# Optimization experiments

Measured on AMD Instinct MI355X. Metric: run time of the kernel, lower is better.

Reference implementation:

```python
import jax, jax.numpy as jnp
import numpy as np
import math

B, S, DM, H = 2, 2048, 1024, 16
DH = DM // H  # 64


def setup_inputs() -> dict:
    key = jax.random.key(0)
    ks = jax.random.split(key, 12)
    s = 1.0 / math.sqrt(DM)
    inp = {
        "key": jax.random.normal(ks[0], (B, S, DM), jnp.float32),
        "value": jax.random.normal(ks[1], (B, S, DM), jnp.float32),
        "query": jax.random.normal(ks[2], (B, S, DM), jnp.float32),
        # causal mask: True = masked out (matches masked_fill semantics)
        "mask": jnp.broadcast_to(~jnp.tril(jnp.ones((S, S), bool)), (B, S, S)),
        "Wk": jax.random.normal(ks[3], (DM, DM), jnp.float32) * s,
        "bk": jnp.zeros((DM,), jnp.float32),
        "Wv": jax.random.normal(ks[4], (DM, DM), jnp.float32) * s,
        "bv": jnp.zeros((DM,), jnp.float32),
        "Wq": jax.random.normal(ks[5], (DM, DM), jnp.float32) * s,
        "bq": jnp.zeros((DM,), jnp.float32),
        "Wo": jax.random.normal(ks[6], (DM, DM), jnp.float32) * s,
        "bo": jnp.zeros((DM,), jnp.float32),
    }
    return inp


def _split_heads(x):
    # [B, S, H*DH] -> [B, H, S, DH]
    b, s, _ = x.shape
    return x.reshape(b, s, H, DH).transpose(0, 2, 1, 3)


def reference(key, value, query, mask, Wk, bk, Wv, bv, Wq, bq, Wo, bo):
    key_up = _split_heads(key @ Wk.T + bk)      # [B,H,S,DH]
    value_up = _split_heads(value @ Wv.T + bv)  # [B,H,S,DH]
    query_up = _split_heads(query @ Wq.T + bq) / math.sqrt(DH)
    scores = jnp.einsum("bhqd,bhkd->bhqk", query_up, key_up)  # [B,H,S,S]
    scores = jnp.where(mask[:, None, :, :], jnp.float32(-1e18), scores)
    attn = jax.nn.softmax(scores, axis=-1)
    # dropout is identity in eval mode
    context = jnp.einsum("bhqk,bhkd->bhqd", attn, value_up)
    context = context.transpose(0, 2, 1, 3).reshape(key.shape[0], -1, H * DH)
    output = context @ Wo.T + bo                # [B,S,DM]
    top_attn = attn[:, 0, :, :]                 # [B,S,S]
    return output, top_attn
```

## Files before the change

### kernel.cpp

```cpp
#include <hip/hip_runtime.h>
#include <hip/hip_bf16.h>
#include <math.h>

#define B_ 2
#define S_ 2048
#define DM_ 1024
#define H_ 16
#define DH_ 64

using short8 = __attribute__((ext_vector_type(8))) short;
using f32x4  = __attribute__((ext_vector_type(4))) float;

typedef const __attribute__((address_space(1))) void* gas_cvp;
typedef __attribute__((address_space(3))) void* las_vp;

struct CvtJobs {
    const float* in[7];
    ushort* out[7];
    int n[7];
};

__device__ __forceinline__ ushort f2bu(float x) {
    __hip_bfloat16 h = __float2bfloat16(x);
    return *(ushort*)&h;
}

__global__ __launch_bounds__(256) void cvt_bf16(CvtJobs jobs) {
    const int j = blockIdx.y;
    const int n = jobs.n[j];
    const int idx = (blockIdx.x * 256 + threadIdx.x) * 8;
    if (idx >= n) return;
    const float* in = jobs.in[j];
    float4 a = *(const float4*)&in[idx];
    float4 b = *(const float4*)&in[idx + 4];
    ushort u[8];
    u[0] = f2bu(a.x); u[1] = f2bu(a.y); u[2] = f2bu(a.z); u[3] = f2bu(a.w);
    u[4] = f2bu(b.x); u[5] = f2bu(b.y); u[6] = f2bu(b.z); u[7] = f2bu(b.w);
    *(int4*)&jobs.out[j][idx] = *(int4*)u;
}

#define GEMM_STAGE(buf, k0v)                                                   \
    {                                                                          \
        _Pragma("unroll")                                                      \
        for (int i = 0; i < 2; i++) {                                          \
            const int s   = i * 256 + tid;                                     \
            const int c   = s >> 7;                                            \
            const int row = s & 127;                                           \
            __builtin_amdgcn_global_load_lds(                                  \
                (gas_cvp)(Ag + (size_t)(i0 + row) * 1024 + (k0v) + c * 8),     \
                (las_vp)&AsB[buf][0][(i * 256 + w * 64) * 8], 16, 0, 0);       \
            __builtin_amdgcn_global_load_lds(                                  \
                (gas_cvp)(Wg + (size_t)(j0 + row) * 1024 + (k0v) + c * 8),     \
                (las_vp)&AsB[buf][1][(i * 256 + w * 64) * 8], 16, 0, 0);       \
        }                                                                      \
    }

#define GEMM_KLOOP()                                                           \
    {                                                                          \
        int bufc = 0;                                                          \
        GEMM_STAGE(0, 0);                                                      \
        GEMM_STAGE(1, 32);                                                     \
        for (int k0 = 0; k0 < 1024; k0 += 32) {                                \
            if (k0 + 32 < 1024)                                                \
                asm volatile("s_waitcnt vmcnt(4)" ::: "memory");               \
            else                                                               \
                asm volatile("s_waitcnt vmcnt(0)" ::: "memory");               \
            __builtin_amdgcn_s_barrier();                                      \
            if (k0 + 64 < 1024) {                                              \
                const int nb = (bufc + 2 >= 3) ? bufc - 1 : bufc + 2;          \
                GEMM_STAGE(nb, k0 + 64);                                       \
            }                                                                  \
            short8 af[4], bf[4];                                               \
            _Pragma("unroll")                                                  \
            for (int m = 0; m < 4; m++)                                        \
                af[m] = *(const short8*)&AsB[bufc][0][((g << 7) + wm * 64 + m * 16 + lr) * 8]; \
            _Pragma("unroll")                                                  \
            for (int n = 0; n < 4; n++)                                        \
                bf[n] = *(const short8*)&AsB[bufc][1][((g << 7) + wn * 64 + n * 16 + lr) * 8]; \
            _Pragma("unroll")                                                  \
            for (int m = 0; m < 4; m++)                                        \
                _Pragma("unroll")                                              \
                for (int n = 0; n < 4; n++)                                    \
                    acc[m][n] = __builtin_amdgcn_mfma_f32_16x16x32_bf16(       \
                        af[m], bf[n], acc[m][n], 0, 0, 0);                     \
            bufc = (bufc + 1 == 3) ? 0 : bufc + 1;                             \
        }                                                                      \
    }

struct ProjJobs {
    const ushort* A[3];
    const ushort* W[3];
    const float* bias[3];
    ushort* C[3];
    float scale[3];
};

__global__ __launch_bounds__(256) void gemm_proj3(ProjJobs jobs)
{
    __shared__ ushort AsB[3][2][4096];

    const int o   = blockIdx.x;
    const int swz = (o & 7) * 96 + (o >> 3);
    const int z   = swz >> 8;
    const int rem = swz & 255;
    const int by  = rem >> 3;
    const int bx  = rem & 7;

    const ushort* Ag = jobs.A[z];
    const ushort* Wg = jobs.W[z];
    const float* bias = jobs.bias[z];
    ushort* C = jobs.C[z];
    const float scale = jobs.scale[z];

    const int tid  = threadIdx.x;
    const int w    = tid >> 6;
    const int lane = tid & 63;
    const int g    = lane >> 4;
    const int lr   = lane & 15;
    const int wm   = w >> 1;
    const int wn   = w & 1;
    const int i0   = by * 128;
    const int j0   = bx * 128;

    f32x4 acc[4][4];
    #pragma unroll
    for (int m = 0; m < 4; m++)
        #pragma unroll
        for (int n = 0; n < 4; n++)
            #pragma unroll
            for (int jj = 0; jj < 4; jj++) acc[m][n][jj] = 0.f;

    GEMM_KLOOP();

    const int colbase = j0 + wn * 64;
    const int rowbase = i0 + wm * 64;
    #pragma unroll
    for (int n = 0; n < 4; n++) {
        const int col = colbase + n * 16 + lr;
        const float bb = bias[col];
        const int hh = col >> 6;
        const int d = col & 63;
        #pragma unroll
        for (int m = 0; m < 4; m++) {
            const int rb = rowbase + m * 16 + g * 4;
            #pragma unroll
            for (int jj = 0; jj < 4; jj++) {
                const float v = (acc[m][n][jj] + bb) * scale;
                const int i = rb + jj;
                const int b = i >> 11;
                const int srow = i & 2047;
                C[(((size_t)b * H_ + hh) * S_ + srow) * DH_ + d] = f2bu(v);
            }
        }
    }
}

__global__ __launch_bounds__(256) void flash_mfma(
    const ushort* __restrict__ Qb, const ushort* __restrict__ Kb,
    const ushort* __restrict__ Vb, __hip_bfloat16* __restrict__ ctx,
    float* __restrict__ m0, float* __restrict__ l0)
{
    const int p = blockIdx.x;
    const int h = blockIdx.y;
    const int b = blockIdx.z;
    const int qtA = p, qtB = 31 - p;
    const size_t hoff = ((size_t)b * H_ + h) * S_ * DH_;
    const ushort* Qh = Qb + hoff;
    const ushort* Kh = Kb + hoff;
    const ushort* Vh = Vb + hoff;

    __shared__ ushort Ks[64][72];
    __shared__ ushort Vt[64][72];
    __shared__ ushort Ps[4][16][72];

    const int tid  = threadIdx.x;
    const int w    = tid >> 6;
    const int lane = tid & 63;
    const int g    = lane >> 4;
    const int lr   = lane & 15;
    const int q0A  = qtA * 64 + w * 16;
    const int q0B  = qtB * 64 + w * 16;

    short8 qfA0, qfA1, qfB0, qfB1;
    {
        const ushort* qa = Qh + (size_t)(q0A + lr) * DH_ + g * 8;
        qfA0 = *(const short8*)(qa);
        qfA1 = *(const short8*)(qa + 32);
        const ushort* qb = Qh + (size_t)(q0B + lr) * DH_ + g * 8;
        qfB0 = *(const short8*)(qb);
        qfB1 = *(const short8*)(qb + 32);
    }

    f32x4 oA[4], oB[4];
    #pragma unroll
    for (int nc = 0; nc < 4; nc++) {
        oA[nc][0]=0.f; oA[nc][1]=0.f; oA[nc][2]=0.f; oA[nc][3]=0.f;
        oB[nc][0]=0.f; oB[nc][1]=0.f; oB[nc][2]=0.f; oB[nc][3]=0.f;
    }
    float mA = -1e30f, lA = 0.f;
    float mB = -1e30f, lB = 0.f;

    const int nkt = qtB + 1;
    const int c0 = w, c1 = w + 4;

    int4 pk0, pk1, pv0, pv1;
    pk0 = *(const int4*)(Kh + (size_t)lane * DH_ + c0 * 8);
    pk1 = *(const int4*)(Kh + (size_t)lane * DH_ + c1 * 8);
    pv0 = *(const int4*)(Vh + (size_t)lane * DH_ + c0 * 8);
    pv1 = *(const int4*)(Vh + (size_t)lane * DH_ + c1 * 8);

    for (int kt = 0; kt < nkt; kt++) {
        const int kvb = kt * 64;
        __syncthreads();
        {
            *(int4*)&Ks[lane][c0 * 8] = pk0;
            *(int4*)&Ks[lane][c1 * 8] = pk1;
            ushort vv[8];
            *(int4*)vv = pv0;
            #pragma unroll
            for (int j2 = 0; j2 < 8; j2++) Vt[c0 * 8 + j2][lane] = vv[j2];
            *(int4*)vv = pv1;
            #pragma unroll
            for (int j2 = 0; j2 < 8; j2++) Vt[c1 * 8 + j2][lane] = vv[j2];
        }
        if (kt + 1 < nkt) {
            const size_t roff = (size_t)(kvb + 64 + lane) * DH_;
            pk0 = *(const int4*)(Kh + roff + c0 * 8);
            pk1 = *(const int4*)(Kh + roff + c1 * 8);
            pv0 = *(const int4*)(Vh + roff + c0 * 8);
            pv1 = *(const int4*)(Vh + roff + c1 * 8);
        }
        __syncthreads();

        #pragma unroll
        for (int u = 0; u < 2; u++) {
            if (u == 0 && kt > qtA) continue;
            const int qt_u  = (u == 0) ? qtA : qtB;
            const int q0w   = (u == 0) ? q0A : q0B;
            const short8 qf0 = (u == 0) ? qfA0 : qfB0;
            const short8 qf1 = (u == 0) ? qfA1 : qfB1;
            float& m_r = (u == 0) ? mA : mB;
            float& l_r = (u == 0) ? lA : lB;
            f32x4* o   = (u == 0) ? oA : oB;
            const int qglob = q0w + lr;

            f32x4 st[4];
            #pragma unroll
            for (int mt = 0; mt < 4; mt++) { st[mt][0]=0.f; st[mt][1]=0.f; st[mt][2]=0.f; st[mt][3]=0.f; }
            __builtin_amdgcn_s_setprio(1);
            #pragma unroll
            for (int mt = 0; mt < 4; mt++) {
                short8 ka = *(const short8*)&Ks[16 * mt + lr][8 * g];
                short8 kb = *(const short8*)&Ks[16 * mt + lr][32 + 8 * g];
                st[mt] = __builtin_amdgcn_mfma_f32_16x16x32_bf16(ka, qf0, st[mt], 0, 0, 0);
                st[mt] = __builtin_amdgcn_mfma_f32_16x16x32_bf16(kb, qf1, st[mt], 0, 0, 0);
            }
            __builtin_amdgcn_s_setprio(0);

            if (kt == qt_u) {
                #pragma unroll
                for (int mt = 0; mt < 4; mt++)
                    #pragma unroll
                    for (int jj = 0; jj < 4; jj++)
                        if (kvb + 16 * mt + 4 * g + jj > qglob) st[mt][jj] = -1e30f;
            }

            float pmax = st[0][0];
            #pragma unroll
            for (int mt = 0; mt < 4; mt++)
                #pragma unroll
                for (int jj = 0; jj < 4; jj++)
                    pmax = fmaxf(pmax, st[mt][jj]);
            pmax = fmaxf(pmax, __shfl_xor(pmax, 16));
            pmax = fmaxf(pmax, __shfl_xor(pmax, 32));

            const bool defer = __all(pmax - m_r <= 8.0f);
            float mnew = m_r, scv = 1.0f;
            if (!defer) {
                mnew = fmaxf(m_r, pmax);
                scv  = __expf(m_r - mnew);
            }

            float lsum = 0.f;
            #pragma unroll
            for (int mt = 0; mt < 4; mt++)
                #pragma unroll
                for (int jj = 0; jj < 4; jj++) {
                    st[mt][jj] = __expf(st[mt][jj] - mnew);
                    lsum += st[mt][jj];
                }
            lsum += __shfl_xor(lsum, 16);
            lsum += __shfl_xor(lsum, 32);
            l_r = l_r * scv + lsum;
            m_r = mnew;

            if (!defer) {
                float sc0 = __shfl(scv, 4 * g + 0);
                float sc1 = __shfl(scv, 4 * g + 1);
                float sc2 = __shfl(scv, 4 * g + 2);
                float sc3 = __shfl(scv, 4 * g + 3);
                #pragma unroll
                for (int nc = 0; nc < 4; nc++) {
                    o[nc][0] *= sc0; o[nc][1] *= sc1;
                    o[nc][2] *= sc2; o[nc][3] *= sc3;
                }
            }

            #pragma unroll
            for (int mt = 0; mt < 4; mt++) {
                ushort u4[4];
                #pragma unroll
                for (int jj = 0; jj < 4; jj++) u4[jj] = f2bu(st[mt][jj]);
                *(uint2*)&Ps[w][lr][16 * mt + 4 * g] = *(uint2*)u4;
            }

            short8 pa0 = *(const short8*)&Ps[w][lr][8 * g];
            short8 pa1 = *(const short8*)&Ps[w][lr][32 + 8 * g];
            __builtin_amdgcn_s_setprio(1);
            #pragma unroll
            for (int nc = 0; nc < 4; nc++) {
                short8 v0 = *(const short8*)&Vt[16 * nc + lr][8 * g];
                short8 v1 = *(const short8*)&Vt[16 * nc + lr][32 + 8 * g];
                o[nc] = __builtin_amdgcn_mfma_f32_16x16x32_bf16(pa0, v0, o[nc], 0, 0, 0);
                o[nc] = __builtin_amdgcn_mfma_f32_16x16x32_bf16(pa1, v1, o[nc], 0, 0, 0);
            }
            __builtin_amdgcn_s_setprio(0);
        }
    }

    #pragma unroll
    for (int u = 0; u < 2; u++) {
        const int q0w = (u == 0) ? q0A : q0B;
        const float m_r = (u == 0) ? mA : mB;
        const float l_r = (u == 0) ? lA : lB;
        const f32x4* o  = (u == 0) ? oA : oB;
        const float linv = 1.0f / l_r;
        float li0 = __shfl(linv, 4 * g + 0);
        float li1 = __shfl(linv, 4 * g + 1);
        float li2 = __shfl(linv, 4 * g + 2);
        float li3 = __shfl(linv, 4 * g + 3);
        #pragma unroll
        for (int reg = 0; reg < 4; reg++) {
            const int qrow = q0w + 4 * g + reg;
            const float li = (reg == 0) ? li0 : (reg == 1) ? li1 : (reg == 2) ? li2 : li3;
            __hip_bfloat16* cp = ctx + ((size_t)b * S_ + qrow) * DM_ + h * DH_;
            #pragma unroll
            for (int nc = 0; nc < 4; nc++)
                cp[16 * nc + lr] = __float2bfloat16(o[nc][reg] * li);
        }
        if (h == 0 && lane < 16) {
            m0[b * S_ + q0w + lane] = m_r;
            l0[b * S_ + q0w + lane] = l_r;
        }
    }
}

__global__ __launch_bounds__(256) void tail_fused(
    const ushort* __restrict__ ctxb, const ushort* __restrict__ Wg_,
    const float* __restrict__ bo, float* __restrict__ out,
    const ushort* __restrict__ Qb, const ushort* __restrict__ Kb,
    const float* __restrict__ m0, const float* __restrict__ l0,
    float* __restrict__ attn)
{
    __shared__ ushort AsB[3][2][4096];
    const int o = blockIdx.x;
    const int tid = threadIdx.x;
    const int w    = tid >> 6;
    const int lane = tid & 63;
    const int g    = lane >> 4;
    const int lr   = lane & 15;

    if (o < 256) {
        const int swz = (o & 7) * 32 + (o >> 3);
        const int by  = swz >> 3;
        const int bx  = swz & 7;
        const int wm  = w >> 1;
        const int wn  = w & 1;
        const int i0  = by * 128;
        const int j0  = bx * 128;
        const ushort* Ag = ctxb;
        const ushort* Wg = Wg_;

        f32x4 acc[4][4];
        #pragma unroll
        for (int m = 0; m < 4; m++)
            #pragma unroll
            for (int n = 0; n < 4; n++)
                #pragma unroll
                for (int jj = 0; jj < 4; jj++) acc[m][n][jj] = 0.f;

        GEMM_KLOOP();

        const int colbase = j0 + wn * 64;
        const int rowbase = i0 + wm * 64;
        #pragma unroll
        for (int n = 0; n < 4; n++) {
            const int col = colbase + n * 16 + lr;
            const float bb = bo[col];
            #pragma unroll
            for (int m = 0; m < 4; m++) {
                const int rb = rowbase + m * 16 + g * 4;
                #pragma unroll
                for (int jj = 0; jj < 4; jj++)
                    out[(size_t)(rb + jj) * DM_ + col] = acc[m][n][jj] + bb;
            }
        }
        return;
    }

    const int t   = o - 256;
    const int kt  = t & 31;
    const int qt2 = (t >> 5) & 31;
    const int b   = t >> 10;
    float* ap = attn + (size_t)b * S_ * S_;

    if (kt > qt2) {
        const int row = qt2 * 64 + (tid >> 2);
        const int col = kt * 64 + (tid & 3) * 16;
        float4 z = {0.f, 0.f, 0.f, 0.f};
        float* rp = ap + (size_t)row * S_ + col;
        *(float4*)&rp[0]  = z;
        *(float4*)&rp[4]  = z;
        *(float4*)&rp[8]  = z;
        *(float4*)&rp[12] = z;
        return;
    }

    ushort (*Ks)[72] = (ushort(*)[72])&AsB[0][0][0];
    const int q0w = qt2 * 64 + w * 16;
    const int kvb = kt * 64;
    const size_t hoff = (size_t)b * H_ * S_ * DH_;
    const ushort* Qh = Qb + hoff;
    const ushort* Kh = Kb + hoff;

    #pragma unroll
    for (int i = 0; i < 2; i++) {
        const int c = w + 4 * i;
        int4 k4 = *(const int4*)(Kh + (size_t)(kvb + lane) * DH_ + c * 8);
        *(int4*)&Ks[lane][c * 8] = k4;
    }

    short8 qf0, qf1;
    {
        const ushort* qp = Qh + (size_t)(q0w + lr) * DH_ + g * 8;
        qf0 = *(const short8*)(qp);
        qf1 = *(const short8*)(qp + 32);
    }
    const int qglob = q0w + lr;
    const float mv   = m0[b * S_ + qglob];
    const float linv = 1.0f / l0[b * S_ + qglob];
    __syncthreads();

    f32x4 st[4];
    #pragma unroll
    for (int mt = 0; mt < 4; mt++) { st[mt][0]=0.f; st[mt][1]=0.f; st[mt][2]=0.f; st[mt][3]=0.f; }
    #pragma unroll
    for (int mt = 0; mt < 4; mt++) {
        short8 ka = *(const short8*)&Ks[16 * mt + lr][8 * g];
        short8 kb = *(const short8*)&Ks[16 * mt + lr][32 + 8 * g];
        st[mt] = __builtin_amdgcn_mfma_f32_16x16x32_bf16(ka, qf0, st[mt], 0, 0, 0);
        st[mt] = __builtin_amdgcn_mfma_f32_16x16x32_bf16(kb, qf1, st[mt], 0, 0, 0);
    }

    float* rowp = ap + (size_t)qglob * S_ + kvb;
    #pragma unroll
    for (int mt = 0; mt < 4; mt++) {
        float4 ov;
        float v[4];
        #pragma unroll
        for (int jj = 0; jj < 4; jj++) {
            const int kv = 16 * mt + 4 * g + jj;
            float pv = __expf(st[mt][jj] - mv) * linv;
            v[jj] = (kvb + kv > qglob) ? 0.f : pv;
        }
        ov.x = v[0]; ov.y = v[1]; ov.z = v[2]; ov.w = v[3];
        *(float4*)&rowp[16 * mt + 4 * g] = ov;
    }
}

extern "C" void kernel_launch(void* const* d_in, const int* in_sizes, int n_in,
                              void* d_out, int out_size, void* d_ws, size_t ws_size,
                              hipStream_t stream)
{
    const float* key   = (const float*)d_in[0];
    const float* value = (const float*)d_in[1];
    const float* query = (const float*)d_in[2];
    const float* Wk = (const float*)d_in[4];
    const float* bk = (const float*)d_in[5];
    const float* Wv = (const float*)d_in[6];
    const float* bv = (const float*)d_in[7];
    const float* Wq = (const float*)d_in[8];
    const float* bq = (const float*)d_in[9];
    const float* Wo = (const float*)d_in[10];
    const float* bo = (const float*)d_in[11];

    char* ws = (char*)d_ws;
    const size_t per = (size_t)B_ * H_ * S_ * DH_;
    const size_t wsz = (size_t)DM_ * DM_;
    __hip_bfloat16* Qp   = (__hip_bfloat16*)ws;
    __hip_bfloat16* Kp   = Qp + per;
    __hip_bfloat16* Vp   = Kp + per;
    __hip_bfloat16* ctxb = Vp + per;
    __hip_bfloat16* qc   = ctxb + per;
    __hip_bfloat16* kc   = qc + per;
    __hip_bfloat16* vc   = kc + per;
    __hip_bfloat16* wqb  = vc + per;
    __hip_bfloat16* wkb  = wqb + wsz;
    __hip_bfloat16* wvb  = wkb + wsz;
    __hip_bfloat16* wob  = wvb + wsz;
    float* m0 = (float*)(wob + wsz);
    float* l0 = m0 + B_ * S_;

    float* out   = (float*)d_out;
    float* topat = out + (size_t)B_ * S_ * DM_;

    CvtJobs jobs;
    jobs.in[0] = query; jobs.out[0] = (ushort*)qc;  jobs.n[0] = (int)per;
    jobs.in[1] = key;   jobs.out[1] = (ushort*)kc;  jobs.n[1] = (int)per;
    jobs.in[2] = value; jobs.out[2] = (ushort*)vc;  jobs.n[2] = (int)per;
    jobs.in[3] = Wq;    jobs.out[3] = (ushort*)wqb; jobs.n[3] = (int)wsz;
    jobs.in[4] = Wk;    jobs.out[4] = (ushort*)wkb; jobs.n[4] = (int)wsz;
    jobs.in[5] = Wv;    jobs.out[5] = (ushort*)wvb; jobs.n[5] = (int)wsz;
    jobs.in[6] = Wo;    jobs.out[6] = (ushort*)wob; jobs.n[6] = (int)wsz;
    cvt_bf16<<<dim3(2048, 7), 256, 0, stream>>>(jobs);

    ProjJobs pj;
    pj.A[0] = (const ushort*)qc; pj.W[0] = (const ushort*)wqb; pj.bias[0] = bq;
    pj.C[0] = (ushort*)Qp; pj.scale[0] = 0.125f;
    pj.A[1] = (const ushort*)kc; pj.W[1] = (const ushort*)wkb; pj.bias[1] = bk;
    pj.C[1] = (ushort*)Kp; pj.scale[1] = 1.0f;
    pj.A[2] = (const ushort*)vc; pj.W[2] = (const ushort*)wvb; pj.bias[2] = bv;
    pj.C[2] = (ushort*)Vp; pj.scale[2] = 1.0f;
    gemm_proj3<<<768, 256, 0, stream>>>(pj);

    flash_mfma<<<dim3(16, H_, B_), 256, 0, stream>>>(
        (const ushort*)Qp, (const ushort*)Kp, (const ushort*)Vp, ctxb, m0, l0);

    tail_fused<<<256 + B_ * 32 * 32, 256, 0, stream>>>(
        (const ushort*)ctxb, (const ushort*)wob, bo, out,
        (const ushort*)Qp, (const ushort*)Kp, m0, l0, topat);
}
```

Measured before the change: 153.7 us.

## Load GEMM MFMA operands directly from global memory, dropping LDS staging

Replaces the triple-buffered global_load_lds pipeline in the projection and output GEMMs with direct per-lane global loads of MFMA fragments, with no barriers or shared memory. The tail kernel's shared memory shrinks to just the K tile, which may let more blocks fit per CU. The cost is that operands are no longer shared through LDS, so each wave re-fetches data its neighbours also use, relying on L1/L2 caching, and load latency is exposed without an explicit software pipeline.

```diff
diff --git a/kernel.cpp b/kernel.cpp
--- a/kernel.cpp
+++ b/kernel.cpp
@@ -10,9 +10,6 @@
 
 using short8 = __attribute__((ext_vector_type(8))) short;
 using f32x4  = __attribute__((ext_vector_type(4))) float;
-
-typedef const __attribute__((address_space(1))) void* gas_cvp;
-typedef __attribute__((address_space(3))) void* las_vp;
 
 struct CvtJobs {
     const float* in[7];
@@ -39,51 +36,23 @@
     *(int4*)&jobs.out[j][idx] = *(int4*)u;
 }
 
-#define GEMM_STAGE(buf, k0v)                                                   \
+#define GEMM_KLOOP_DIRECT()                                                    \
     {                                                                          \
-        _Pragma("unroll")                                                      \
-        for (int i = 0; i < 2; i++) {                                          \
-            const int s   = i * 256 + tid;                                     \
-            const int c   = s >> 7;                                            \
-            const int row = s & 127;                                           \
-            __builtin_amdgcn_global_load_lds(                                  \
-                (gas_cvp)(Ag + (size_t)(i0 + row) * 1024 + (k0v) + c * 8),     \
-                (las_vp)&AsB[buf][0][(i * 256 + w * 64) * 8], 16, 0, 0);       \
-            __builtin_amdgcn_global_load_lds(                                  \
-                (gas_cvp)(Wg + (size_t)(j0 + row) * 1024 + (k0v) + c * 8),     \
-                (las_vp)&AsB[buf][1][(i * 256 + w * 64) * 8], 16, 0, 0);       \
-        }                                                                      \
-    }
-
-#define GEMM_KLOOP()                                                           \
-    {                                                                          \
-        int bufc = 0;                                                          \
-        GEMM_STAGE(0, 0);                                                      \
-        GEMM_STAGE(1, 32);                                                     \
+        _Pragma("unroll 2")                                                    \
         for (int k0 = 0; k0 < 1024; k0 += 32) {                                \
-            if (k0 + 32 < 1024)                                                \
-                asm volatile("s_waitcnt vmcnt(4)" ::: "memory");               \
-            else                                                               \
-                asm volatile("s_waitcnt vmcnt(0)" ::: "memory");               \
-            __builtin_amdgcn_s_barrier();                                      \
-            if (k0 + 64 < 1024) {                                              \
-                const int nb = (bufc + 2 >= 3) ? bufc - 1 : bufc + 2;          \
-                GEMM_STAGE(nb, k0 + 64);                                       \
-            }                                                                  \
             short8 af[4], bf[4];                                               \
             _Pragma("unroll")                                                  \
             for (int m = 0; m < 4; m++)                                        \
-                af[m] = *(const short8*)&AsB[bufc][0][((g << 7) + wm * 64 + m * 16 + lr) * 8]; \
+                af[m] = *(const short8*)(pa[m] + k0);                          \
             _Pragma("unroll")                                                  \
             for (int n = 0; n < 4; n++)                                        \
-                bf[n] = *(const short8*)&AsB[bufc][1][((g << 7) + wn * 64 + n * 16 + lr) * 8]; \
+                bf[n] = *(const short8*)(pb[n] + k0);                          \
             _Pragma("unroll")                                                  \
             for (int m = 0; m < 4; m++)                                        \
                 _Pragma("unroll")                                              \
                 for (int n = 0; n < 4; n++)                                    \
                     acc[m][n] = __builtin_amdgcn_mfma_f32_16x16x32_bf16(       \
                         af[m], bf[n], acc[m][n], 0, 0, 0);                     \
-            bufc = (bufc + 1 == 3) ? 0 : bufc + 1;                             \
         }                                                                      \
     }
 
@@ -97,8 +66,6 @@
 
 __global__ __launch_bounds__(256) void gemm_proj3(ProjJobs jobs)
 {
-    __shared__ ushort AsB[3][2][4096];
-
     const int o   = blockIdx.x;
     const int swz = (o & 7) * 96 + (o >> 3);
     const int z   = swz >> 8;
@@ -122,6 +89,15 @@
     const int i0   = by * 128;
     const int j0   = bx * 128;
 
+    const ushort* pa[4];
+    const ushort* pb[4];
+    #pragma unroll
+    for (int m = 0; m < 4; m++)
+        pa[m] = Ag + (size_t)(i0 + wm * 64 + m * 16 + lr) * 1024 + g * 8;
+    #pragma unroll
+    for (int n = 0; n < 4; n++)
+        pb[n] = Wg + (size_t)(j0 + wn * 64 + n * 16 + lr) * 1024 + g * 8;
+
     f32x4 acc[4][4];
     #pragma unroll
     for (int m = 0; m < 4; m++)
@@ -130,7 +106,7 @@
             #pragma unroll
             for (int jj = 0; jj < 4; jj++) acc[m][n][jj] = 0.f;
 
-    GEMM_KLOOP();
+    GEMM_KLOOP_DIRECT();
 
     const int colbase = j0 + wn * 64;
     const int rowbase = i0 + wm * 64;
@@ -362,7 +338,7 @@
     const float* __restrict__ m0, const float* __restrict__ l0,
     float* __restrict__ attn)
 {
-    __shared__ ushort AsB[3][2][4096];
+    __shared__ ushort Ks_sh[64][72];
     const int o = blockIdx.x;
     const int tid = threadIdx.x;
     const int w    = tid >> 6;
@@ -378,8 +354,15 @@
         const int wn  = w & 1;
         const int i0  = by * 128;
         const int j0  = bx * 128;
-        const ushort* Ag = ctxb;
-        const ushort* Wg = Wg_;
+
+        const ushort* pa[4];
+        const ushort* pb[4];
+        #pragma unroll
+        for (int m = 0; m < 4; m++)
+            pa[m] = ctxb + (size_t)(i0 + wm * 64 + m * 16 + lr) * 1024 + g * 8;
+        #pragma unroll
+        for (int n = 0; n < 4; n++)
+            pb[n] = Wg_ + (size_t)(j0 + wn * 64 + n * 16 + lr) * 1024 + g * 8;
 
         f32x4 acc[4][4];
         #pragma unroll
@@ -389,7 +372,7 @@
                 #pragma unroll
                 for (int jj = 0; jj < 4; jj++) acc[m][n][jj] = 0.f;
 
-        GEMM_KLOOP();
+        GEMM_KLOOP_DIRECT();
 
         const int colbase = j0 + wn * 64;
         const int rowbase = i0 + wm * 64;
@@ -426,7 +409,6 @@
         return;
     }
 
-    ushort (*Ks)[72] = (ushort(*)[72])&AsB[0][0][0];
     const int q0w = qt2 * 64 + w * 16;
     const int kvb = kt * 64;
     const size_t hoff = (size_t)b * H_ * S_ * DH_;
@@ -437,7 +419,7 @@
     for (int i = 0; i < 2; i++) {
         const int c = w + 4 * i;
         int4 k4 = *(const int4*)(Kh + (size_t)(kvb + lane) * DH_ + c * 8);
-        *(int4*)&Ks[lane][c * 8] = k4;
+        *(int4*)&Ks_sh[lane][c * 8] = k4;
     }
 
     short8 qf0, qf1;
@@ -456,8 +438,8 @@
     for (int mt = 0; mt < 4; mt++) { st[mt][0]=0.f; st[mt][1]=0.f; st[mt][2]=0.f; st[mt][3]=0.f; }
     #pragma unroll
     for (int mt = 0; mt < 4; mt++) {
-        short8 ka = *(const short8*)&Ks[16 * mt + lr][8 * g];
-        short8 kb = *(const short8*)&Ks[16 * mt + lr][32 + 8 * g];
+        short8 ka = *(const short8*)&Ks_sh[16 * mt + lr][8 * g];
+        short8 kb = *(const short8*)&Ks_sh[16 * mt + lr][32 + 8 * g];
         st[mt] = __builtin_amdgcn_mfma_f32_16x16x32_bf16(ka, qf0, st[mt], 0, 0, 0);
         st[mt] = __builtin_amdgcn_mfma_f32_16x16x32_bf16(kb, qf1, st[mt], 0, 0, 0);
     }
```

Result: slower. 200.6 us (+30.5%).

## Enlarge GEMM tiles to 256x128 with 512-thread blocks and pair attention tiles

Applied to the files above, without the earlier changes.

The projection and output GEMMs now use 512-thread blocks that compute 256x128 tiles, sharing each staged W tile across twice as many A rows and halving the block count. The top-attention part of the fused tail kernel now packs two 64x64 score tiles into each 512-thread block, and the K-tile load and barrier are restructured so masked and unmasked halves can coexist. This is meant to reduce redundant W loads and per-block overhead, at the cost of fewer blocks and possibly lower occupancy from the larger shared-memory and thread footprint.

```diff
diff --git a/kernel.cpp b/kernel.cpp
--- a/kernel.cpp
+++ b/kernel.cpp
@@ -39,44 +39,50 @@
     *(int4*)&jobs.out[j][idx] = *(int4*)u;
 }
 
-#define GEMM_STAGE(buf, k0v)                                                   \
+#define STAGE512(buf, k0v)                                                     \
     {                                                                          \
         _Pragma("unroll")                                                      \
         for (int i = 0; i < 2; i++) {                                          \
-            const int s   = i * 256 + tid;                                     \
-            const int c   = s >> 7;                                            \
-            const int row = s & 127;                                           \
+            const int s   = i * 512 + tid;                                     \
+            const int c   = s >> 8;                                            \
+            const int row = s & 255;                                           \
             __builtin_amdgcn_global_load_lds(                                  \
                 (gas_cvp)(Ag + (size_t)(i0 + row) * 1024 + (k0v) + c * 8),     \
-                (las_vp)&AsB[buf][0][(i * 256 + w * 64) * 8], 16, 0, 0);       \
+                (las_vp)&SH[(buf) * 12288 + (i * 512 + w * 64) * 8], 16, 0, 0);\
+        }                                                                      \
+        {                                                                      \
+            const int c   = tid >> 7;                                          \
+            const int row = tid & 127;                                         \
             __builtin_amdgcn_global_load_lds(                                  \
                 (gas_cvp)(Wg + (size_t)(j0 + row) * 1024 + (k0v) + c * 8),     \
-                (las_vp)&AsB[buf][1][(i * 256 + w * 64) * 8], 16, 0, 0);       \
+                (las_vp)&SH[(buf) * 12288 + 8192 + (w * 64) * 8], 16, 0, 0);   \
         }                                                                      \
     }
 
-#define GEMM_KLOOP()                                                           \
+#define GEMM_KLOOP512()                                                        \
     {                                                                          \
         int bufc = 0;                                                          \
-        GEMM_STAGE(0, 0);                                                      \
-        GEMM_STAGE(1, 32);                                                     \
+        STAGE512(0, 0);                                                        \
+        STAGE512(1, 32);                                                       \
         for (int k0 = 0; k0 < 1024; k0 += 32) {                                \
             if (k0 + 32 < 1024)                                                \
-                asm volatile("s_waitcnt vmcnt(4)" ::: "memory");               \
+                asm volatile("s_waitcnt vmcnt(3)" ::: "memory");               \
             else                                                               \
                 asm volatile("s_waitcnt vmcnt(0)" ::: "memory");               \
             __builtin_amdgcn_s_barrier();                                      \
             if (k0 + 64 < 1024) {                                              \
                 const int nb = (bufc + 2 >= 3) ? bufc - 1 : bufc + 2;          \
-                GEMM_STAGE(nb, k0 + 64);                                       \
+                STAGE512(nb, k0 + 64);                                         \
             }                                                                  \
             short8 af[4], bf[4];                                               \
             _Pragma("unroll")                                                  \
             for (int m = 0; m < 4; m++)                                        \
-                af[m] = *(const short8*)&AsB[bufc][0][((g << 7) + wm * 64 + m * 16 + lr) * 8]; \
+                af[m] = *(const short8*)&SH[bufc * 12288 +                     \
+                    ((g << 8) + wm * 64 + m * 16 + lr) * 8];                   \
             _Pragma("unroll")                                                  \
             for (int n = 0; n < 4; n++)                                        \
-                bf[n] = *(const short8*)&AsB[bufc][1][((g << 7) + wn * 64 + n * 16 + lr) * 8]; \
+                bf[n] = *(const short8*)&SH[bufc * 12288 + 8192 +              \
+                    ((g << 7) + wn * 64 + n * 16 + lr) * 8];                   \
             _Pragma("unroll")                                                  \
             for (int m = 0; m < 4; m++)                                        \
                 _Pragma("unroll")                                              \
@@ -95,14 +101,14 @@
     float scale[3];
 };
 
-__global__ __launch_bounds__(256) void gemm_proj3(ProjJobs jobs)
+__global__ __launch_bounds__(512) void gemm_proj3(ProjJobs jobs)
 {
-    __shared__ ushort AsB[3][2][4096];
+    __shared__ ushort SH[36864];
 
     const int o   = blockIdx.x;
-    const int swz = (o & 7) * 96 + (o >> 3);
-    const int z   = swz >> 8;
-    const int rem = swz & 255;
+    const int swz = (o & 7) * 48 + (o >> 3);
+    const int z   = swz >> 7;
+    const int rem = swz & 127;
     const int by  = rem >> 3;
     const int bx  = rem & 7;
 
@@ -119,7 +125,7 @@
     const int lr   = lane & 15;
     const int wm   = w >> 1;
     const int wn   = w & 1;
-    const int i0   = by * 128;
+    const int i0   = by * 256;
     const int j0   = bx * 128;
 
     f32x4 acc[4][4];
@@ -130,7 +136,7 @@
             #pragma unroll
             for (int jj = 0; jj < 4; jj++) acc[m][n][jj] = 0.f;
 
-    GEMM_KLOOP();
+    GEMM_KLOOP512();
 
     const int colbase = j0 + wn * 64;
     const int rowbase = i0 + wm * 64;
@@ -355,14 +361,14 @@
     }
 }
 
-__global__ __launch_bounds__(256) void tail_fused(
+__global__ __launch_bounds__(512) void tail_fused(
     const ushort* __restrict__ ctxb, const ushort* __restrict__ Wg_,
     const float* __restrict__ bo, float* __restrict__ out,
     const ushort* __restrict__ Qb, const ushort* __restrict__ Kb,
     const float* __restrict__ m0, const float* __restrict__ l0,
     float* __restrict__ attn)
 {
-    __shared__ ushort AsB[3][2][4096];
+    __shared__ ushort SH[36864];
     const int o = blockIdx.x;
     const int tid = threadIdx.x;
     const int w    = tid >> 6;
@@ -370,13 +376,13 @@
     const int g    = lane >> 4;
     const int lr   = lane & 15;
 
-    if (o < 256) {
-        const int swz = (o & 7) * 32 + (o >> 3);
+    if (o < 128) {
+        const int swz = (o & 7) * 16 + (o >> 3);
         const int by  = swz >> 3;
         const int bx  = swz & 7;
         const int wm  = w >> 1;
         const int wn  = w & 1;
-        const int i0  = by * 128;
+        const int i0  = by * 256;
         const int j0  = bx * 128;
         const ushort* Ag = ctxb;
         const ushort* Wg = Wg_;
@@ -389,7 +395,7 @@
                 #pragma unroll
                 for (int jj = 0; jj < 4; jj++) acc[m][n][jj] = 0.f;
 
-        GEMM_KLOOP();
+        GEMM_KLOOP512();
 
         const int colbase = j0 + wn * 64;
         const int rowbase = i0 + wm * 64;
@@ -408,15 +414,36 @@
         return;
     }
 
-    const int t   = o - 256;
+    const int sub = w >> 2;
+    const int wl  = w & 3;
+    const int t   = (o - 128) * 2 + sub;
     const int kt  = t & 31;
     const int qt2 = (t >> 5) & 31;
     const int b   = t >> 10;
     float* ap = attn + (size_t)b * S_ * S_;
-
-    if (kt > qt2) {
-        const int row = qt2 * 64 + (tid >> 2);
-        const int col = kt * 64 + (tid & 3) * 16;
+    const bool masked = (kt > qt2);
+
+    ushort (*Ks)[72] = (ushort(*)[72])&SH[sub * 4608];
+    const int q0w = qt2 * 64 + wl * 16;
+    const int kvb = kt * 64;
+    const size_t hoff = (size_t)b * H_ * S_ * DH_;
+    const ushort* Qh = Qb + hoff;
+    const ushort* Kh = Kb + hoff;
+
+    if (!masked) {
+        #pragma unroll
+        for (int i = 0; i < 2; i++) {
+            const int c = wl + 4 * i;
+            int4 k4 = *(const int4*)(Kh + (size_t)(kvb + lane) * DH_ + c * 8);
+            *(int4*)&Ks[lane][c * 8] = k4;
+        }
+    }
+    __syncthreads();
+
+    if (masked) {
+        const int lt  = tid & 255;
+        const int row = qt2 * 64 + (lt >> 2);
+        const int col = kt * 64 + (lt & 3) * 16;
         float4 z = {0.f, 0.f, 0.f, 0.f};
         float* rp = ap + (size_t)row * S_ + col;
         *(float4*)&rp[0]  = z;
@@ -426,20 +453,6 @@
         return;
     }
 
-    ushort (*Ks)[72] = (ushort(*)[72])&AsB[0][0][0];
-    const int q0w = qt2 * 64 + w * 16;
-    const int kvb = kt * 64;
-    const size_t hoff = (size_t)b * H_ * S_ * DH_;
-    const ushort* Qh = Qb + hoff;
-    const ushort* Kh = Kb + hoff;
-
-    #pragma unroll
-    for (int i = 0; i < 2; i++) {
-        const int c = w + 4 * i;
-        int4 k4 = *(const int4*)(Kh + (size_t)(kvb + lane) * DH_ + c * 8);
-        *(int4*)&Ks[lane][c * 8] = k4;
-    }
-
     short8 qf0, qf1;
     {
         const ushort* qp = Qh + (size_t)(q0w + lr) * DH_ + g * 8;
@@ -449,7 +462,6 @@
     const int qglob = q0w + lr;
     const float mv   = m0[b * S_ + qglob];
     const float linv = 1.0f / l0[b * S_ + qglob];
-    __syncthreads();
 
     f32x4 st[4];
     #pragma unroll
@@ -531,12 +543,12 @@
     pj.C[1] = (ushort*)Kp; pj.scale[1] = 1.0f;
     pj.A[2] = (const ushort*)vc; pj.W[2] = (const ushort*)wvb; pj.bias[2] = bv;
     pj.C[2] = (ushort*)Vp; pj.scale[2] = 1.0f;
-    gemm_proj3<<<768, 256, 0, stream>>>(pj);
+    gemm_proj3<<<384, 512, 0, stream>>>(pj);
 
     flash_mfma<<<dim3(16, H_, B_), 256, 0, stream>>>(
         (const ushort*)Qp, (const ushort*)Kp, (const ushort*)Vp, ctxb, m0, l0);
 
-    tail_fused<<<256 + B_ * 32 * 32, 256, 0, stream>>>(
+    tail_fused<<<128 + B_ * 32 * 32 / 2, 512, 0, stream>>>(
         (const ushort*)ctxb, (const ushort*)wob, bo, out,
         (const ushort*)Qp, (const ushort*)Kp, m0, l0, topat);
 }
```

After: 167.2 us. +8.8%, slower.

## Split flash attention into 32-row query tiles, one tile per wave pair

Applied to the files above, without the earlier changes.

Each flash attention block now handles two 32-row query tiles taken from opposite ends of the causal range, with each wave owning 16 rows, where it used to process two 64-row tiles sequentially per wave. The grid doubles to 32 blocks per head, so per-wave register state halves and more blocks can be resident. Waves whose rows finish early skip compute but still join the shared K/V loads and barriers, so some waves sit idle within a block. The causal mask is applied on each wave's own last key tile.

```diff
diff --git a/kernel.cpp b/kernel.cpp
--- a/kernel.cpp
+++ b/kernel.cpp
@@ -160,10 +160,9 @@
     const ushort* __restrict__ Vb, __hip_bfloat16* __restrict__ ctx,
     float* __restrict__ m0, float* __restrict__ l0)
 {
-    const int p = blockIdx.x;
+    const int j = blockIdx.x;
     const int h = blockIdx.y;
     const int b = blockIdx.z;
-    const int qtA = p, qtB = 31 - p;
     const size_t hoff = ((size_t)b * H_ + h) * S_ * DH_;
     const ushort* Qh = Qb + hoff;
     const ushort* Kh = Kb + hoff;
@@ -178,29 +177,26 @@
     const int lane = tid & 63;
     const int g    = lane >> 4;
     const int lr   = lane & 15;
-    const int q0A  = qtA * 64 + w * 16;
-    const int q0B  = qtB * 64 + w * 16;
-
-    short8 qfA0, qfA1, qfB0, qfB1;
+    const int side = w >> 1;
+    const int sub  = w & 1;
+    const int qt32 = side ? (63 - j) : j;
+    const int q0w  = qt32 * 32 + sub * 16;
+    const int qglob = q0w + lr;
+    const int myNkt = (q0w + 15) / 64 + 1;
+    const int nkt   = (65 - j) / 2;
+
+    short8 qf0, qf1;
     {
-        const ushort* qa = Qh + (size_t)(q0A + lr) * DH_ + g * 8;
-        qfA0 = *(const short8*)(qa);
-        qfA1 = *(const short8*)(qa + 32);
-        const ushort* qb = Qh + (size_t)(q0B + lr) * DH_ + g * 8;
-        qfB0 = *(const short8*)(qb);
-        qfB1 = *(const short8*)(qb + 32);
-    }
-
-    f32x4 oA[4], oB[4];
-    #pragma unroll
-    for (int nc = 0; nc < 4; nc++) {
-        oA[nc][0]=0.f; oA[nc][1]=0.f; oA[nc][2]=0.f; oA[nc][3]=0.f;
-        oB[nc][0]=0.f; oB[nc][1]=0.f; oB[nc][2]=0.f; oB[nc][3]=0.f;
-    }
-    float mA = -1e30f, lA = 0.f;
-    float mB = -1e30f, lB = 0.f;
-
-    const int nkt = qtB + 1;
+        const ushort* qp = Qh + (size_t)(q0w + lr) * DH_ + g * 8;
+        qf0 = *(const short8*)(qp);
+        qf1 = *(const short8*)(qp + 32);
+    }
+
+    f32x4 o[4];
+    #pragma unroll
+    for (int nc = 0; nc < 4; nc++) { o[nc][0]=0.f; o[nc][1]=0.f; o[nc][2]=0.f; o[nc][3]=0.f; }
+    float m_r = -1e30f, l_r = 0.f;
+
     const int c0 = w, c1 = w + 4;
 
     int4 pk0, pk1, pv0, pv1;
@@ -232,18 +228,7 @@
         }
         __syncthreads();
 
-        #pragma unroll
-        for (int u = 0; u < 2; u++) {
-            if (u == 0 && kt > qtA) continue;
-            const int qt_u  = (u == 0) ? qtA : qtB;
-            const int q0w   = (u == 0) ? q0A : q0B;
-            const short8 qf0 = (u == 0) ? qfA0 : qfB0;
-            const short8 qf1 = (u == 0) ? qfA1 : qfB1;
-            float& m_r = (u == 0) ? mA : mB;
-            float& l_r = (u == 0) ? lA : lB;
-            f32x4* o   = (u == 0) ? oA : oB;
-            const int qglob = q0w + lr;
-
+        if (kt < myNkt) {
             f32x4 st[4];
             #pragma unroll
             for (int mt = 0; mt < 4; mt++) { st[mt][0]=0.f; st[mt][1]=0.f; st[mt][2]=0.f; st[mt][3]=0.f; }
@@ -257,7 +242,7 @@
             }
             __builtin_amdgcn_s_setprio(0);
 
-            if (kt == qt_u) {
+            if (kt == myNkt - 1) {
                 #pragma unroll
                 for (int mt = 0; mt < 4; mt++)
                     #pragma unroll
@@ -328,12 +313,7 @@
         }
     }
 
-    #pragma unroll
-    for (int u = 0; u < 2; u++) {
-        const int q0w = (u == 0) ? q0A : q0B;
-        const float m_r = (u == 0) ? mA : mB;
-        const float l_r = (u == 0) ? lA : lB;
-        const f32x4* o  = (u == 0) ? oA : oB;
+    {
         const float linv = 1.0f / l_r;
         float li0 = __shfl(linv, 4 * g + 0);
         float li1 = __shfl(linv, 4 * g + 1);
@@ -533,7 +513,7 @@
     pj.C[2] = (ushort*)Vp; pj.scale[2] = 1.0f;
     gemm_proj3<<<768, 256, 0, stream>>>(pj);
 
-    flash_mfma<<<dim3(16, H_, B_), 256, 0, stream>>>(
+    flash_mfma<<<dim3(32, H_, B_), 256, 0, stream>>>(
         (const ushort*)Qp, (const ushort*)Kp, (const ushort*)Vp, ctxb, m0, l0);
 
     tail_fused<<<256 + B_ * 32 * 32, 256, 0, stream>>>(
```

Measured after the change: 176.9 us. +15.1%, slower.
